# Optimization experiments

Hardware: AMD Instinct MI355X
Metric: run time of the kernel (lower is better)

Reference implementation:

```python
import jax, jax.numpy as jnp
import numpy as np

B, S, P, D, H = 2, 1024, 1024, 2048, 16
DH = D // H
QMAX = 127.0


def quantize(x):
    # per-tensor abs-max int8 quantization, matching torch quantize(bits=8)
    scale = jnp.max(jnp.abs(x)) / QMAX
    x_q = jnp.clip(jnp.round(x / scale), -128.0, 127.0).astype(jnp.int8)
    return x_q, scale


def dequantize(x_q, scale):
    return x_q.astype(jnp.float32) * scale


def setup_inputs() -> dict:
    key = jax.random.key(0)
    ks = jax.random.split(key, 12)
    sd = 1.0 / np.sqrt(D)
    inp = {
        'hidden_states': jax.random.normal(ks[0], (B, S, D), jnp.float32),
        'Wq': jax.random.normal(ks[1], (D, D), jnp.float32) * sd,
        'bq': jnp.zeros((D,), jnp.float32),
        'Wk': jax.random.normal(ks[2], (D, D), jnp.float32) * sd,
        'bk': jnp.zeros((D,), jnp.float32),
        'Wv': jax.random.normal(ks[3], (D, D), jnp.float32) * sd,
        'bv': jnp.zeros((D,), jnp.float32),
        'Wo': jax.random.normal(ks[4], (D, D), jnp.float32) * sd,
        'bo': jnp.zeros((D,), jnp.float32),
        'past_k_q': jax.random.randint(ks[5], (B, P, D), -128, 128).astype(jnp.int8),
        'past_k_scale': jnp.float32(0.03),
        'past_v_q': jax.random.randint(ks[6], (B, P, D), -128, 128).astype(jnp.int8),
        'past_v_scale': jnp.float32(0.02),
    }
    return inp


def attention(h, k, v, Wq, bq, Wo, bo):
    # standard causal MHA; query positions are offset by the cache length P
    T = k.shape[1]  # P + S
    q = (h @ Wq + bq).reshape(B, S, H, DH)
    kh = k.reshape(B, T, H, DH)
    vh = v.reshape(B, T, H, DH)
    scores = jnp.einsum('bshd,bthd->bhst', q, kh) / np.sqrt(DH)  # [B,H,S,T]
    causal = jnp.arange(T)[None, :] <= (P + jnp.arange(S))[:, None]  # [S,T]
    scores = jnp.where(causal[None, None], scores, jnp.float32(-1e30))
    attn = jax.nn.softmax(scores, axis=-1)
    out = jnp.einsum('bhst,bthd->bshd', attn, vh).reshape(B, S, D)
    return out @ Wo + bo


def reference(hidden_states, Wq, bq, Wk, bk, Wv, bv, Wo, bo,
              past_k_q, past_k_scale, past_v_q, past_v_scale):
    k = hidden_states @ Wk + bk  # [B,S,D]
    v = hidden_states @ Wv + bv
    k_q, k_scale = quantize(k)
    v_q, v_scale = quantize(v)
    # dequantize cached KV and concat along the sequence dim (dim=1)
    k_prev = dequantize(past_k_q, past_k_scale)
    v_prev = dequantize(past_v_q, past_v_scale)
    k_full = jnp.concatenate([k_prev, k], axis=1)  # [B,P+S,D]
    v_full = jnp.concatenate([v_prev, v], axis=1)
    out = attention(hidden_states, k_full, v_full, Wq, bq, Wo, bo)
    return out, k_q, k_scale, v_q, v_scale
```

## Files before the change

kernel.cpp:

```cpp
#include <hip/hip_runtime.h>

#define SOFT_SCALE 0.08838834764831845f
#define BSD 4194304
#define NELEM 4194304

typedef __attribute__((ext_vector_type(4))) float    f32x4;
typedef __attribute__((ext_vector_type(8))) short    bf16x8;
typedef __attribute__((ext_vector_type(4))) short    bf16x4;
typedef __attribute__((ext_vector_type(4))) unsigned u32x4;

__device__ __forceinline__ float bs2f(short s) {
    unsigned u = ((unsigned)(unsigned short)s) << 16;
    return __builtin_bit_cast(float, u);
}
__device__ __forceinline__ short f2bs(float f) {
    unsigned u = __builtin_bit_cast(unsigned, f);
    unsigned r = (u + 0x7fffu + ((u >> 16) & 1u)) >> 16;
    return (short)r;
}

__device__ __forceinline__ void stage16(const short* g, short* l) {
#if __has_builtin(__builtin_amdgcn_global_load_lds)
    __builtin_amdgcn_global_load_lds(
        (const __attribute__((address_space(1))) void*)g,
        (__attribute__((address_space(3))) void*)l, 16, 0, 0);
#else
    *(bf16x8*)l = *(const bf16x8*)g;
#endif
}

__global__ void probe_init(const int* __restrict__ q, float* __restrict__ scal) {
    const int lane = threadIdx.x;
    int bad = 0;
#pragma unroll
    for (int i = 0; i < 4; ++i) {
        const int v = q[i * 64 + lane];
        bad |= (v < -128 || v > 127) ? 1 : 0;
    }
    const int anybad = __any(bad);
    if (lane == 0) ((int*)scal)[2] = anybad ? 0 : 1;
    if (lane == 1) scal[0] = 0.f;
    if (lane == 2) scal[1] = 0.f;
}

__global__ void conv_bf16(const float* __restrict__ X, short* __restrict__ Y) {
    const int stride = gridDim.x * blockDim.x;
    for (int i = blockIdx.x * blockDim.x + threadIdx.x; i < NELEM / 8; i += stride) {
        const int e = i * 8;
        f32x4 a = *(const f32x4*)&X[e];
        f32x4 b = *(const f32x4*)&X[e + 4];
        bf16x8 o;
        o[0] = f2bs(a[0]); o[1] = f2bs(a[1]); o[2] = f2bs(a[2]); o[3] = f2bs(a[3]);
        o[4] = f2bs(b[0]); o[5] = f2bs(b[1]); o[6] = f2bs(b[2]); o[7] = f2bs(b[3]);
        *(bf16x8*)&Y[e] = o;
    }
}

__global__ __launch_bounds__(256) void transpose_conv(const float* __restrict__ W0,
                                                      const float* __restrict__ W1,
                                                      const float* __restrict__ W2,
                                                      short* __restrict__ WT) {
    __shared__ __align__(16) short Tl[64 * 68];
    const float* W = blockIdx.z == 0 ? W0 : (blockIdx.z == 1 ? W1 : W2);
    short* out = WT + (long)blockIdx.z * 4194304;
    const int tid = threadIdx.x;
    const int n0 = blockIdx.x * 64, k0 = blockIdx.y * 64;
#pragma unroll
    for (int i = 0; i < 4; ++i) {
        const int e = i * 1024 + tid * 4;
        const int r = e >> 6, c = e & 63;
        f32x4 f = *(const f32x4*)&W[(long)(k0 + r) * 2048 + n0 + c];
        bf16x4 s4 = { f2bs(f[0]), f2bs(f[1]), f2bs(f[2]), f2bs(f[3]) };
        *(bf16x4*)&Tl[r * 68 + c] = s4;
    }
    __syncthreads();
#pragma unroll
    for (int i = 0; i < 4; ++i) {
        const int e = i * 1024 + tid * 4;
        const int nr = e >> 6, kk = e & 63;
        bf16x4 o = { Tl[(kk + 0) * 68 + nr], Tl[(kk + 1) * 68 + nr],
                     Tl[(kk + 2) * 68 + nr], Tl[(kk + 3) * 68 + nr] };
        *(bf16x4*)&out[(long)(n0 + nr) * 2048 + k0 + kk] = o;
    }
}

__global__ void dequant_kernel(const void* __restrict__ pk, const void* __restrict__ pv,
                               const float* __restrict__ psk, const float* __restrict__ psv,
                               short* __restrict__ Kf, short* __restrict__ Vf,
                               const int* __restrict__ wsflag) {
    const int z = blockIdx.z;
    const void* src = z ? pv : pk;
    const float sc = z ? *psv : *psk;
    short* dst = z ? Vf : Kf;
    const int flag = wsflag[2];
    const int stride = gridDim.x * blockDim.x;
    for (int i = blockIdx.x * blockDim.x + threadIdx.x; i < NELEM / 8; i += stride) {
        const int e = i * 8;
        int vals[8];
        if (flag) {
            const int* s = (const int*)src + e;
            *(int4*)&vals[0] = *(const int4*)&s[0];
            *(int4*)&vals[4] = *(const int4*)&s[4];
        } else {
            const int2 wv = *(const int2*)((const char*)src + e);
#pragma unroll
            for (int j = 0; j < 4; ++j) vals[j] = (int)(signed char)(wv.x >> (8 * j));
#pragma unroll
            for (int j = 0; j < 4; ++j) vals[4 + j] = (int)(signed char)(wv.y >> (8 * j));
        }
        bf16x8 o;
#pragma unroll
        for (int j = 0; j < 8; ++j) o[j] = f2bs((float)vals[j] * sc);
        *(bf16x8*)&dst[e + ((e >> 21) << 21)] = o;
    }
}

__global__ __launch_bounds__(256, 2) void gemm_m97(
    const short* __restrict__ A,
    const short* __restrict__ Bt0, const short* __restrict__ Bt1, const short* __restrict__ Bt2,
    const float* __restrict__ bi0, const float* __restrict__ bi1, const float* __restrict__ bi2,
    void* __restrict__ o0, void* __restrict__ o1, void* __restrict__ o2,
    int mode_sgl, float scale_sgl) {
    __shared__ __align__(16) short Al[2][4096];
    __shared__ __align__(16) short Bl[2][4096];
    const int nbx = gridDim.x, nby = gridDim.y, nbz = gridDim.z;
    const int nwg = nbx * nby * nbz;
    const int orig = blockIdx.x + nbx * (blockIdx.y + nby * blockIdx.z);
    const int cpx = nwg >> 3;
    int swz = (orig & 7) * cpx + (orig >> 3);
    const int bx = swz % nbx; swz /= nbx;
    const int by = swz % nby;
    const int bz = swz / nby;

    const short* Bt   = bz == 0 ? Bt0 : (bz == 1 ? Bt1 : Bt2);
    const float* bias = bz == 0 ? bi0 : (bz == 1 ? bi1 : bi2);
    void* outp        = bz == 0 ? o0  : (bz == 1 ? o1  : o2);
    int mode; float scl;
    if (nbz == 3) { mode = (bz == 0) ? 1 : 2; scl = (bz == 0) ? SOFT_SCALE : 1.f; }
    else          { mode = mode_sgl;          scl = scale_sgl; }

    const int tid = threadIdx.x, lane = tid & 63, w = tid >> 6;
    const int wm = w >> 1, wn = w & 1, l4 = lane >> 4, ln = lane & 15;
    const int m0 = by * 128, n0 = bx * 128;

    const short* gA0 = A  + (long)(m0 + (tid >> 2)) * 2048 + (tid & 3) * 8;
    const short* gA1 = gA0 + 64 * 2048;
    const short* gB0 = Bt + (long)(n0 + (tid >> 2)) * 2048 + (tid & 3) * 8;
    const short* gB1 = gB0 + 64 * 2048;

    f32x4 acc[4][4];
#pragma unroll
    for (int mi = 0; mi < 4; ++mi)
#pragma unroll
        for (int ni = 0; ni < 4; ++ni) acc[mi][ni] = (f32x4){0, 0, 0, 0};

#define STAGE_G(buf, ko)                                   \
    do {                                                   \
        stage16(gA0 + (ko), &Al[buf][tid * 8]);            \
        stage16(gA1 + (ko), &Al[buf][2048 + tid * 8]);     \
        stage16(gB0 + (ko), &Bl[buf][tid * 8]);            \
        stage16(gB1 + (ko), &Bl[buf][2048 + tid * 8]);     \
    } while (0)

    STAGE_G(0, 0);
    asm volatile("s_waitcnt vmcnt(0)" ::: "memory");
    __syncthreads();
    int cur = 0;
    for (int kt = 0; kt < 64; ++kt) {
        if (kt < 63) STAGE_G(cur ^ 1, (kt + 1) * 32);
        bf16x8 af[4], bfr[4];
#pragma unroll
        for (int mi = 0; mi < 4; ++mi)
            af[mi] = *(const bf16x8*)&Al[cur][(wm * 64 + mi * 16 + ln) * 32 + l4 * 8];
#pragma unroll
        for (int ni = 0; ni < 4; ++ni)
            bfr[ni] = *(const bf16x8*)&Bl[cur][(wn * 64 + ni * 16 + ln) * 32 + l4 * 8];
#pragma unroll
        for (int mi = 0; mi < 4; ++mi)
#pragma unroll
            for (int ni = 0; ni < 4; ++ni)
                acc[mi][ni] = __builtin_amdgcn_mfma_f32_16x16x32_bf16(
                    af[mi], bfr[ni], acc[mi][ni], 0, 0, 0);
        asm volatile("s_waitcnt vmcnt(0)" ::: "memory");
        __syncthreads();
        cur ^= 1;
    }
#undef STAGE_G

#pragma unroll
    for (int ni = 0; ni < 4; ++ni) {
        const int gn = n0 + wn * 64 + ni * 16 + ln;
        const float bv = bias[gn];
#pragma unroll
        for (int mi = 0; mi < 4; ++mi) {
#pragma unroll
            for (int r = 0; r < 4; ++r) {
                const int gm = m0 + wm * 64 + mi * 16 + l4 * 4 + r;
                const float v = (acc[mi][ni][r] + bv) * scl;
                if (mode == 0) {
                    ((float*)outp)[(long)gm * 2048 + gn] = v;
                } else if (mode == 1) {
                    ((short*)outp)[(long)gm * 2048 + gn] = f2bs(v);
                } else {
                    const int gr = gm + 1024 + ((gm >> 10) << 10);
                    ((short*)outp)[(long)gr * 2048 + gn] = f2bs(v);
                }
            }
        }
    }
}

__global__ void absmax_kernel(const short* __restrict__ Kf, const short* __restrict__ Vf,
                              float* __restrict__ scal) {
    const int z = blockIdx.z;
    const short* src = z ? Vf : Kf;
    const int tid = threadIdx.x, lane = tid & 63, w = tid >> 6;
    float mx = 0.f;
    const int stride = gridDim.x * blockDim.x;
    for (int i = blockIdx.x * blockDim.x + tid; i < NELEM / 8; i += stride) {
        const int e = i * 8;
        const int flat = e + 2097152 + ((e >> 21) << 21);
        bf16x8 v = *(const bf16x8*)&src[flat];
#pragma unroll
        for (int j = 0; j < 8; ++j) mx = fmaxf(mx, fabsf(bs2f(v[j])));
    }
#pragma unroll
    for (int o = 32; o > 0; o >>= 1) mx = fmaxf(mx, __shfl_xor(mx, o));
    __shared__ float wred[4];
    if (lane == 0) wred[w] = mx;
    __syncthreads();
    if (tid == 0) {
        const float m2 = fmaxf(fmaxf(wred[0], wred[1]), fmaxf(wred[2], wred[3]));
        atomicMax((unsigned int*)&scal[z], __builtin_bit_cast(unsigned int, m2));
    }
}

__global__ void quantize_kernel(const short* __restrict__ Kf, const short* __restrict__ Vf,
                                const float* __restrict__ scal, float* __restrict__ out) {
    const int z = blockIdx.z;
    const short* src = z ? Vf : Kf;
    const float mx = scal[z];
    const float scale = mx * (1.f / 127.f);
    const float inv = (mx > 0.f) ? 127.f / mx : 0.f;
    const long ob = z ? (2L * BSD + 1) : (1L * BSD);
    if (blockIdx.x == 0 && threadIdx.x == 0)
        out[z ? (3L * BSD + 1) : (2L * BSD)] = scale;
    const int stride = gridDim.x * blockDim.x;
    for (int i = blockIdx.x * blockDim.x + threadIdx.x; i < NELEM; i += stride) {
        const int flat = i + 2097152 + ((i >> 21) << 21);
        const float x = bs2f(src[flat]);
        float q = rintf(x * inv);
        q = fminf(127.f, fmaxf(-128.f, q));
        out[ob + i] = q;
    }
}

__global__ __launch_bounds__(256, 2) void attn_kernel(const short* __restrict__ Q,
                                                      const short* __restrict__ Kf,
                                                      const short* __restrict__ Vf,
                                                      short* __restrict__ O) {
    __shared__ __align__(16) short Kl[64 * 136];
    __shared__ __align__(16) short Vt[128 * 72];
    const int b = blockIdx.z, h = blockIdx.y;
    const int qt = (b == 0) ? blockIdx.x : (15 - blockIdx.x);
    const int tid = threadIdx.x, w = tid >> 6, lane = tid & 63;
    const int l4 = lane >> 4, n = lane & 15;
    const int rg = tid >> 4, cg = tid & 15, stc = cg * 8;
    const int sIdx = qt * 64 + w * 16 + n;
    const int qlim = 1024 + sIdx;

    bf16x8 qf[4];
#pragma unroll
    for (int c = 0; c < 4; ++c)
        qf[c] = *(const bf16x8*)&Q[(long)(b * 1024 + sIdx) * 2048 + h * 128 + c * 32 + l4 * 8];

    f32x4 acco[8];
#pragma unroll
    for (int i = 0; i < 8; ++i) acco[i] = (f32x4){0, 0, 0, 0};
    float m_run = -1e30f, l_run = 0.f;

    const short* Kb = Kf + (long)(b * 2048) * 2048 + h * 128;
    const short* Vb = Vf + (long)(b * 2048) * 2048 + h * 128;
    const int nt = 17 + qt;

    bf16x8 kreg[4], vreg[4];
#pragma unroll
    for (int i = 0; i < 4; ++i) kreg[i] = *(const bf16x8*)&Kb[(long)(i * 16 + rg) * 2048 + stc];
#pragma unroll
    for (int i = 0; i < 4; ++i) vreg[i] = *(const bf16x8*)&Vb[(long)(rg * 4 + i) * 2048 + stc];

    for (int t = 0; t < nt; ++t) {
        const int t0 = t * 64;
        __syncthreads();
#pragma unroll
        for (int i = 0; i < 4; ++i)
            *(bf16x8*)&Kl[(i * 16 + rg) * 136 + stc] = kreg[i];
#pragma unroll
        for (int j = 0; j < 8; ++j) {
            const int d = stc + j;
            bf16x4 c4 = { vreg[0][j], vreg[1][j], vreg[2][j], vreg[3][j] };
            *(bf16x4*)&Vt[d * 72 + ((rg ^ ((d >> 3) & 7)) << 2)] = c4;
        }
        if (t + 1 < nt) {
            const int t1 = (t + 1) * 64;
#pragma unroll
            for (int i = 0; i < 4; ++i)
                kreg[i] = *(const bf16x8*)&Kb[(long)(t1 + i * 16 + rg) * 2048 + stc];
#pragma unroll
            for (int i = 0; i < 4; ++i)
                vreg[i] = *(const bf16x8*)&Vb[(long)(t1 + rg * 4 + i) * 2048 + stc];
        }
        __syncthreads();

        float p[16];
        __builtin_amdgcn_s_setprio(1);
#pragma unroll
        for (int kt = 0; kt < 4; ++kt) {
            f32x4 sc4 = (f32x4){0, 0, 0, 0};
#pragma unroll
            for (int c = 0; c < 4; ++c) {
                bf16x8 kfr = *(const bf16x8*)&Kl[(kt * 16 + n) * 136 + c * 32 + l4 * 8];
                sc4 = __builtin_amdgcn_mfma_f32_16x16x32_bf16(kfr, qf[c], sc4, 0, 0, 0);
            }
#pragma unroll
            for (int r = 0; r < 4; ++r) {
                const int kg = t0 + kt * 16 + l4 * 4 + r;
                p[kt * 4 + r] = (kg <= qlim) ? sc4[r] : -1e30f;
            }
        }
        __builtin_amdgcn_s_setprio(0);

        float tmax = p[0];
#pragma unroll
        for (int i = 1; i < 16; ++i) tmax = fmaxf(tmax, p[i]);
        tmax = fmaxf(tmax, __shfl_xor(tmax, 16));
        tmax = fmaxf(tmax, __shfl_xor(tmax, 32));
        const float mnew = fmaxf(m_run, tmax);
        const float fac = __expf(m_run - mnew);
        float tsum = 0.f;
#pragma unroll
        for (int i = 0; i < 16; ++i) { p[i] = __expf(p[i] - mnew); tsum += p[i]; }
        tsum += __shfl_xor(tsum, 16);
        tsum += __shfl_xor(tsum, 32);
        l_run = l_run * fac + tsum;
        m_run = mnew;
#pragma unroll
        for (int i = 0; i < 8; ++i) acco[i] *= fac;

        u32x4 pw0, pw1;
#pragma unroll
        for (int wd = 0; wd < 4; ++wd) {
            unsigned r0, r1;
            asm("v_cvt_pk_bf16_f32 %0, %1, %2" : "=v"(r0) : "v"(p[2 * wd]), "v"(p[2 * wd + 1]));
            asm("v_cvt_pk_bf16_f32 %0, %1, %2" : "=v"(r1) : "v"(p[8 + 2 * wd]), "v"(p[8 + 2 * wd + 1]));
            pw0[wd] = r0; pw1[wd] = r1;
        }
        bf16x8 pb[2] = { __builtin_bit_cast(bf16x8, pw0), __builtin_bit_cast(bf16x8, pw1) };

        __builtin_amdgcn_s_setprio(1);
#pragma unroll
        for (int dc = 0; dc < 8; ++dc) {
            const int d = dc * 16 + n;
            const int swd = ((d >> 3) & 7) << 2;
#pragma unroll
            for (int k32 = 0; k32 < 2; ++k32) {
                bf16x4 g0 = *(const bf16x4*)&Vt[d * 72 + (k32 * 32 + ((4 * l4) ^ swd))];
                bf16x4 g1 = *(const bf16x4*)&Vt[d * 72 + (k32 * 32 + ((16 + 4 * l4) ^ swd))];
                bf16x8 vf = { g0[0], g0[1], g0[2], g0[3], g1[0], g1[1], g1[2], g1[3] };
                acco[dc] = __builtin_amdgcn_mfma_f32_16x16x32_bf16(vf, pb[k32], acco[dc], 0, 0, 0);
            }
        }
        __builtin_amdgcn_s_setprio(0);
    }

    __syncthreads();
    const float inv = 1.f / l_run;
#pragma unroll
    for (int dc = 0; dc < 8; ++dc)
#pragma unroll
        for (int r = 0; r < 4; ++r)
            Kl[(w * 16 + n) * 136 + dc * 16 + l4 * 4 + r] = f2bs(acco[dc][r] * inv);
    __syncthreads();
#pragma unroll
    for (int i = 0; i < 4; ++i) {
        const int row = i * 4 + (lane >> 4);
        const int col = (lane & 15) * 8;
        bf16x8 ov = *(const bf16x8*)&Kl[(w * 16 + row) * 136 + col];
        *(bf16x8*)&O[(long)(b * 1024 + qt * 64 + w * 16 + row) * 2048 + h * 128 + col] = ov;
    }
}

extern "C" void kernel_launch(void* const* d_in, const int* in_sizes, int n_in,
                              void* d_out, int out_size, void* d_ws, size_t ws_size,
                              hipStream_t stream) {
    const float* h   = (const float*)d_in[0];
    const float* Wq  = (const float*)d_in[1];
    const float* bq  = (const float*)d_in[2];
    const float* Wk  = (const float*)d_in[3];
    const float* bk  = (const float*)d_in[4];
    const float* Wv  = (const float*)d_in[5];
    const float* bv  = (const float*)d_in[6];
    const float* Wo  = (const float*)d_in[7];
    const float* bo  = (const float*)d_in[8];
    const void*  pkq = d_in[9];
    const float* pks = (const float*)d_in[10];
    const void*  pvq = d_in[11];
    const float* pvs = (const float*)d_in[12];
    float* out = (float*)d_out;

    char* ws = (char*)d_ws;
    dim3 blk(256);
    dim3 tr_grid(32, 32);
    const bool big = (ws_size >= 75500000ull);

    if (big) {
        float* scal  = (float*)ws;
        short* hbf   = (short*)(ws + 256);
        short* WT3   = (short*)(ws + 256 + 1L * 8388608);
        short* Qbf   = (short*)(ws + 256 + 4L * 8388608);
        short* Kfull = (short*)(ws + 256 + 5L * 8388608);
        short* Vfull = (short*)(ws + 256 + 5L * 8388608 + 16777216);
        short* attnb = hbf;

        probe_init<<<1, 64, 0, stream>>>((const int*)pkq, scal);
        conv_bf16<<<1024, blk, 0, stream>>>(h, hbf);
        dequant_kernel<<<dim3(256, 1, 2), blk, 0, stream>>>(pkq, pvq, pks, pvs, Kfull, Vfull,
                                                            (const int*)d_ws);
        transpose_conv<<<dim3(32, 32, 3), blk, 0, stream>>>(Wq, Wk, Wv, WT3);
        gemm_m97<<<dim3(16, 16, 3), blk, 0, stream>>>(hbf, WT3, WT3 + 4194304, WT3 + 8388608,
                                                      bq, bk, bv, Qbf, Kfull, Vfull, 0, 1.f);
        absmax_kernel<<<dim3(512, 1, 2), blk, 0, stream>>>(Kfull, Vfull, scal);
        quantize_kernel<<<dim3(512, 1, 2), blk, 0, stream>>>(Kfull, Vfull, scal, out);
        attn_kernel<<<dim3(16, 16, 2), blk, 0, stream>>>(Qbf, Kfull, Vfull, attnb);
        transpose_conv<<<dim3(32, 32, 1), blk, 0, stream>>>(Wo, Wo, Wo, WT3);
        gemm_m97<<<dim3(16, 16, 1), blk, 0, stream>>>(attnb, WT3, WT3, WT3, bo, bo, bo,
                                                      out, out, out, 0, 1.f);
    } else {
        float* scal  = (float*)ws;
        short* hbf   = (short*)(ws + 256);
        short* WT    = (short*)(ws + 256 + 1L * 8388608);
        short* Qbf   = (short*)(ws + 256 + 2L * 8388608);
        short* Kfull = (short*)(ws + 256 + 3L * 8388608);
        short* Vfull = (short*)(ws + 256 + 3L * 8388608 + 16777216);
        short* attnb = hbf;

        probe_init<<<1, 64, 0, stream>>>((const int*)pkq, scal);
        conv_bf16<<<1024, blk, 0, stream>>>(h, hbf);
        dequant_kernel<<<dim3(256, 1, 2), blk, 0, stream>>>(pkq, pvq, pks, pvs, Kfull, Vfull,
                                                            (const int*)d_ws);
        transpose_conv<<<dim3(32, 32, 1), blk, 0, stream>>>(Wk, Wk, Wk, WT);
        gemm_m97<<<dim3(16, 16, 1), blk, 0, stream>>>(hbf, WT, WT, WT, bk, bk, bk,
                                                      Kfull, Kfull, Kfull, 2, 1.f);
        transpose_conv<<<dim3(32, 32, 1), blk, 0, stream>>>(Wv, Wv, Wv, WT);
        gemm_m97<<<dim3(16, 16, 1), blk, 0, stream>>>(hbf, WT, WT, WT, bv, bv, bv,
                                                      Vfull, Vfull, Vfull, 2, 1.f);
        absmax_kernel<<<dim3(512, 1, 2), blk, 0, stream>>>(Kfull, Vfull, scal);
        quantize_kernel<<<dim3(512, 1, 2), blk, 0, stream>>>(Kfull, Vfull, scal, out);
        transpose_conv<<<dim3(32, 32, 1), blk, 0, stream>>>(Wq, Wq, Wq, WT);
        gemm_m97<<<dim3(16, 16, 1), blk, 0, stream>>>(hbf, WT, WT, WT, bq, bq, bq,
                                                      Qbf, Qbf, Qbf, 1, SOFT_SCALE);
        attn_kernel<<<dim3(16, 16, 2), blk, 0, stream>>>(Qbf, Kfull, Vfull, attnb);
        transpose_conv<<<dim3(32, 32, 1), blk, 0, stream>>>(Wo, Wo, Wo, WT);
        gemm_m97<<<dim3(16, 16, 1), blk, 0, stream>>>(attnb, WT, WT, WT, bo, bo, bo,
                                                      out, out, out, 0, 1.f);
    }
}
```

Measured before the change: 237.5 us.

## Fuse absmax into GEMM epilogue, deepen GEMM pipeline, tune attention softmax

The separate absmax kernel is removed, and the K/V abs-max is now reduced in the projection GEMM epilogue with a wave shuffle plus atomicMax. The GEMM moves from double to quad LDS buffering with partial vmcnt waits, an XOR swizzle on LDS columns and s_setprio around the MFMAs. Attention gains a new block-to-(head,batch,tile) mapping, skips causal masking on early tiles, and adds a lazy online-softmax rescale with an 8.0 threshold. The quantize kernel is vectorised to four elements per thread. Quad buffering doubles GEMM LDS use, which may reduce occupancy.

```diff
diff --git a/kernel.cpp b/kernel.cpp
--- a/kernel.cpp
+++ b/kernel.cpp
@@ -120,9 +120,9 @@
     const short* __restrict__ Bt0, const short* __restrict__ Bt1, const short* __restrict__ Bt2,
     const float* __restrict__ bi0, const float* __restrict__ bi1, const float* __restrict__ bi2,
     void* __restrict__ o0, void* __restrict__ o1, void* __restrict__ o2,
-    int mode_sgl, float scale_sgl) {
-    __shared__ __align__(16) short Al[2][4096];
-    __shared__ __align__(16) short Bl[2][4096];
+    float* __restrict__ scal, int mode_sgl, float scale_sgl, int amax_sgl) {
+    __shared__ __align__(16) short Al[4][4096];
+    __shared__ __align__(16) short Bl[4][4096];
     const int nbx = gridDim.x, nby = gridDim.y, nbz = gridDim.z;
     const int nwg = nbx * nby * nbz;
     const int orig = blockIdx.x + nbx * (blockIdx.y + nby * blockIdx.z);
@@ -135,17 +135,20 @@
     const short* Bt   = bz == 0 ? Bt0 : (bz == 1 ? Bt1 : Bt2);
     const float* bias = bz == 0 ? bi0 : (bz == 1 ? bi1 : bi2);
     void* outp        = bz == 0 ? o0  : (bz == 1 ? o1  : o2);
-    int mode; float scl;
-    if (nbz == 3) { mode = (bz == 0) ? 1 : 2; scl = (bz == 0) ? SOFT_SCALE : 1.f; }
-    else          { mode = mode_sgl;          scl = scale_sgl; }
+    int mode, amx; float scl;
+    if (nbz == 3) { mode = (bz == 0) ? 1 : 2; scl = (bz == 0) ? SOFT_SCALE : 1.f;
+                    amx = (bz == 0) ? -1 : (bz - 1); }
+    else          { mode = mode_sgl; scl = scale_sgl; amx = amax_sgl; }
 
     const int tid = threadIdx.x, lane = tid & 63, w = tid >> 6;
     const int wm = w >> 1, wn = w & 1, l4 = lane >> 4, ln = lane & 15;
     const int m0 = by * 128, n0 = bx * 128;
 
-    const short* gA0 = A  + (long)(m0 + (tid >> 2)) * 2048 + (tid & 3) * 8;
+    const int srow = tid >> 2;
+    const int cswz = ((tid & 3) ^ ((srow >> 1) & 3)) * 8;
+    const short* gA0 = A  + (long)(m0 + srow) * 2048 + cswz;
     const short* gA1 = gA0 + 64 * 2048;
-    const short* gB0 = Bt + (long)(n0 + (tid >> 2)) * 2048 + (tid & 3) * 8;
+    const short* gB0 = Bt + (long)(n0 + srow) * 2048 + cswz;
     const short* gB1 = gB0 + 64 * 2048;
 
     f32x4 acc[4][4];
@@ -163,30 +166,37 @@
     } while (0)
 
     STAGE_G(0, 0);
-    asm volatile("s_waitcnt vmcnt(0)" ::: "memory");
-    __syncthreads();
-    int cur = 0;
+    STAGE_G(1, 32);
+    STAGE_G(2, 64);
+
+    const int gsw = (ln >> 1) & 3;
     for (int kt = 0; kt < 64; ++kt) {
-        if (kt < 63) STAGE_G(cur ^ 1, (kt + 1) * 32);
+        if (kt < 62)      asm volatile("s_waitcnt vmcnt(8)" ::: "memory");
+        else if (kt == 62) asm volatile("s_waitcnt vmcnt(4)" ::: "memory");
+        else               asm volatile("s_waitcnt vmcnt(0)" ::: "memory");
+        asm volatile("s_waitcnt lgkmcnt(0)" ::: "memory");
+        __builtin_amdgcn_s_barrier();
+        if (kt < 61) STAGE_G((kt + 3) & 3, (kt + 3) * 32);
+        const int cur = kt & 3;
         bf16x8 af[4], bfr[4];
 #pragma unroll
         for (int mi = 0; mi < 4; ++mi)
-            af[mi] = *(const bf16x8*)&Al[cur][(wm * 64 + mi * 16 + ln) * 32 + l4 * 8];
+            af[mi] = *(const bf16x8*)&Al[cur][(wm * 64 + mi * 16 + ln) * 32 + (l4 ^ gsw) * 8];
 #pragma unroll
         for (int ni = 0; ni < 4; ++ni)
-            bfr[ni] = *(const bf16x8*)&Bl[cur][(wn * 64 + ni * 16 + ln) * 32 + l4 * 8];
+            bfr[ni] = *(const bf16x8*)&Bl[cur][(wn * 64 + ni * 16 + ln) * 32 + (l4 ^ gsw) * 8];
+        __builtin_amdgcn_s_setprio(1);
 #pragma unroll
         for (int mi = 0; mi < 4; ++mi)
 #pragma unroll
             for (int ni = 0; ni < 4; ++ni)
                 acc[mi][ni] = __builtin_amdgcn_mfma_f32_16x16x32_bf16(
                     af[mi], bfr[ni], acc[mi][ni], 0, 0, 0);
-        asm volatile("s_waitcnt vmcnt(0)" ::: "memory");
-        __syncthreads();
-        cur ^= 1;
+        __builtin_amdgcn_s_setprio(0);
     }
 #undef STAGE_G
 
+    float amax = 0.f;
 #pragma unroll
     for (int ni = 0; ni < 4; ++ni) {
         const int gn = n0 + wn * 64 + ni * 16 + ln;
@@ -197,6 +207,7 @@
             for (int r = 0; r < 4; ++r) {
                 const int gm = m0 + wm * 64 + mi * 16 + l4 * 4 + r;
                 const float v = (acc[mi][ni][r] + bv) * scl;
+                amax = fmaxf(amax, fabsf(v));
                 if (mode == 0) {
                     ((float*)outp)[(long)gm * 2048 + gn] = v;
                 } else if (mode == 1) {
@@ -208,30 +219,11 @@
             }
         }
     }
-}
-
-__global__ void absmax_kernel(const short* __restrict__ Kf, const short* __restrict__ Vf,
-                              float* __restrict__ scal) {
-    const int z = blockIdx.z;
-    const short* src = z ? Vf : Kf;
-    const int tid = threadIdx.x, lane = tid & 63, w = tid >> 6;
-    float mx = 0.f;
-    const int stride = gridDim.x * blockDim.x;
-    for (int i = blockIdx.x * blockDim.x + tid; i < NELEM / 8; i += stride) {
-        const int e = i * 8;
-        const int flat = e + 2097152 + ((e >> 21) << 21);
-        bf16x8 v = *(const bf16x8*)&src[flat];
-#pragma unroll
-        for (int j = 0; j < 8; ++j) mx = fmaxf(mx, fabsf(bs2f(v[j])));
-    }
-#pragma unroll
-    for (int o = 32; o > 0; o >>= 1) mx = fmaxf(mx, __shfl_xor(mx, o));
-    __shared__ float wred[4];
-    if (lane == 0) wred[w] = mx;
-    __syncthreads();
-    if (tid == 0) {
-        const float m2 = fmaxf(fmaxf(wred[0], wred[1]), fmaxf(wred[2], wred[3]));
-        atomicMax((unsigned int*)&scal[z], __builtin_bit_cast(unsigned int, m2));
+    if (amx >= 0) {
+#pragma unroll
+        for (int o = 32; o > 0; o >>= 1) amax = fmaxf(amax, __shfl_xor(amax, o));
+        if (lane == 0)
+            atomicMax((unsigned int*)&scal[amx], __builtin_bit_cast(unsigned int, amax));
     }
 }
 
@@ -246,12 +238,16 @@
     if (blockIdx.x == 0 && threadIdx.x == 0)
         out[z ? (3L * BSD + 1) : (2L * BSD)] = scale;
     const int stride = gridDim.x * blockDim.x;
-    for (int i = blockIdx.x * blockDim.x + threadIdx.x; i < NELEM; i += stride) {
-        const int flat = i + 2097152 + ((i >> 21) << 21);
-        const float x = bs2f(src[flat]);
-        float q = rintf(x * inv);
-        q = fminf(127.f, fmaxf(-128.f, q));
-        out[ob + i] = q;
+    for (int i = blockIdx.x * blockDim.x + threadIdx.x; i < NELEM / 4; i += stride) {
+        const int e = i * 4;
+        const int flat = e + 2097152 + ((e >> 21) << 21);
+        bf16x4 x4 = *(const bf16x4*)&src[flat];
+        float4 q;
+        q.x = fminf(127.f, fmaxf(-128.f, rintf(bs2f(x4[0]) * inv)));
+        q.y = fminf(127.f, fmaxf(-128.f, rintf(bs2f(x4[1]) * inv)));
+        q.z = fminf(127.f, fmaxf(-128.f, rintf(bs2f(x4[2]) * inv)));
+        q.w = fminf(127.f, fmaxf(-128.f, rintf(bs2f(x4[3]) * inv)));
+        *(float4*)&out[ob + e] = q;
     }
 }
 
@@ -261,8 +257,13 @@
                                                       short* __restrict__ O) {
     __shared__ __align__(16) short Kl[64 * 136];
     __shared__ __align__(16) short Vt[128 * 72];
-    const int b = blockIdx.z, h = blockIdx.y;
-    const int qt = (b == 0) ? blockIdx.x : (15 - blockIdx.x);
+    const int L = blockIdx.x + 16 * (blockIdx.y + 16 * blockIdx.z);
+    const int x = L & 7, rr = L >> 3;
+    const int qt0 = rr & 15, pgrp = rr >> 4;
+    const int p = x + 8 * pgrp;
+    const int h = p >> 1, b = p & 1;
+    const int qt = (pgrp >= 2) ? (15 - qt0) : qt0;
+
     const int tid = threadIdx.x, w = tid >> 6, lane = tid & 63;
     const int l4 = lane >> 4, n = lane & 15;
     const int rg = tid >> 4, cg = tid & 15, stc = cg * 8;
@@ -312,7 +313,7 @@
         }
         __syncthreads();
 
-        float p[16];
+        float p16[16];
         __builtin_amdgcn_s_setprio(1);
 #pragma unroll
         for (int kt = 0; kt < 4; ++kt) {
@@ -323,36 +324,43 @@
                 sc4 = __builtin_amdgcn_mfma_f32_16x16x32_bf16(kfr, qf[c], sc4, 0, 0, 0);
             }
 #pragma unroll
-            for (int r = 0; r < 4; ++r) {
-                const int kg = t0 + kt * 16 + l4 * 4 + r;
-                p[kt * 4 + r] = (kg <= qlim) ? sc4[r] : -1e30f;
+            for (int r = 0; r < 4; ++r) p16[kt * 4 + r] = sc4[r];
+        }
+        __builtin_amdgcn_s_setprio(0);
+        if (t >= 16) {
+#pragma unroll
+            for (int i = 0; i < 16; ++i) {
+                const int kg = t0 + (i >> 2) * 16 + l4 * 4 + (i & 3);
+                if (kg > qlim) p16[i] = -1e30f;
             }
         }
-        __builtin_amdgcn_s_setprio(0);
-
-        float tmax = p[0];
-#pragma unroll
-        for (int i = 1; i < 16; ++i) tmax = fmaxf(tmax, p[i]);
+
+        float tmax = p16[0];
+#pragma unroll
+        for (int i = 1; i < 16; ++i) tmax = fmaxf(tmax, p16[i]);
         tmax = fmaxf(tmax, __shfl_xor(tmax, 16));
         tmax = fmaxf(tmax, __shfl_xor(tmax, 32));
-        const float mnew = fmaxf(m_run, tmax);
-        const float fac = __expf(m_run - mnew);
+        if (!__all(tmax <= m_run + 8.f)) {
+            const float mnew = fmaxf(m_run, tmax);
+            const float fac = __expf(m_run - mnew);
+            l_run *= fac;
+#pragma unroll
+            for (int i = 0; i < 8; ++i) acco[i] *= fac;
+            m_run = mnew;
+        }
         float tsum = 0.f;
 #pragma unroll
-        for (int i = 0; i < 16; ++i) { p[i] = __expf(p[i] - mnew); tsum += p[i]; }
+        for (int i = 0; i < 16; ++i) { p16[i] = __expf(p16[i] - m_run); tsum += p16[i]; }
         tsum += __shfl_xor(tsum, 16);
         tsum += __shfl_xor(tsum, 32);
-        l_run = l_run * fac + tsum;
-        m_run = mnew;
-#pragma unroll
-        for (int i = 0; i < 8; ++i) acco[i] *= fac;
+        l_run += tsum;
 
         u32x4 pw0, pw1;
 #pragma unroll
         for (int wd = 0; wd < 4; ++wd) {
             unsigned r0, r1;
-            asm("v_cvt_pk_bf16_f32 %0, %1, %2" : "=v"(r0) : "v"(p[2 * wd]), "v"(p[2 * wd + 1]));
-            asm("v_cvt_pk_bf16_f32 %0, %1, %2" : "=v"(r1) : "v"(p[8 + 2 * wd]), "v"(p[8 + 2 * wd + 1]));
+            asm("v_cvt_pk_bf16_f32 %0, %1, %2" : "=v"(r0) : "v"(p16[2 * wd]), "v"(p16[2 * wd + 1]));
+            asm("v_cvt_pk_bf16_f32 %0, %1, %2" : "=v"(r1) : "v"(p16[8 + 2 * wd]), "v"(p16[8 + 2 * wd + 1]));
             pw0[wd] = r0; pw1[wd] = r1;
         }
         bf16x8 pb[2] = { __builtin_bit_cast(bf16x8, pw0), __builtin_bit_cast(bf16x8, pw1) };
@@ -410,7 +418,6 @@
 
     char* ws = (char*)d_ws;
     dim3 blk(256);
-    dim3 tr_grid(32, 32);
     const bool big = (ws_size >= 75500000ull);
 
     if (big) {
@@ -428,13 +435,13 @@
                                                             (const int*)d_ws);
         transpose_conv<<<dim3(32, 32, 3), blk, 0, stream>>>(Wq, Wk, Wv, WT3);
         gemm_m97<<<dim3(16, 16, 3), blk, 0, stream>>>(hbf, WT3, WT3 + 4194304, WT3 + 8388608,
-                                                      bq, bk, bv, Qbf, Kfull, Vfull, 0, 1.f);
-        absmax_kernel<<<dim3(512, 1, 2), blk, 0, stream>>>(Kfull, Vfull, scal);
-        quantize_kernel<<<dim3(512, 1, 2), blk, 0, stream>>>(Kfull, Vfull, scal, out);
+                                                      bq, bk, bv, Qbf, Kfull, Vfull,
+                                                      scal, 0, 1.f, -1);
+        quantize_kernel<<<dim3(256, 1, 2), blk, 0, stream>>>(Kfull, Vfull, scal, out);
         attn_kernel<<<dim3(16, 16, 2), blk, 0, stream>>>(Qbf, Kfull, Vfull, attnb);
         transpose_conv<<<dim3(32, 32, 1), blk, 0, stream>>>(Wo, Wo, Wo, WT3);
         gemm_m97<<<dim3(16, 16, 1), blk, 0, stream>>>(attnb, WT3, WT3, WT3, bo, bo, bo,
-                                                      out, out, out, 0, 1.f);
+                                                      out, out, out, scal, 0, 1.f, -1);
     } else {
         float* scal  = (float*)ws;
         short* hbf   = (short*)(ws + 256);
@@ -450,18 +457,17 @@
                                                             (const int*)d_ws);
         transpose_conv<<<dim3(32, 32, 1), blk, 0, stream>>>(Wk, Wk, Wk, WT);
         gemm_m97<<<dim3(16, 16, 1), blk, 0, stream>>>(hbf, WT, WT, WT, bk, bk, bk,
-                                                      Kfull, Kfull, Kfull, 2, 1.f);
+                                                      Kfull, Kfull, Kfull, scal, 2, 1.f, 0);
         transpose_conv<<<dim3(32, 32, 1), blk, 0, stream>>>(Wv, Wv, Wv, WT);
         gemm_m97<<<dim3(16, 16, 1), blk, 0, stream>>>(hbf, WT, WT, WT, bv, bv, bv,
-                                                      Vfull, Vfull, Vfull, 2, 1.f);
-        absmax_kernel<<<dim3(512, 1, 2), blk, 0, stream>>>(Kfull, Vfull, scal);
-        quantize_kernel<<<dim3(512, 1, 2), blk, 0, stream>>>(Kfull, Vfull, scal, out);
+                                                      Vfull, Vfull, Vfull, scal, 2, 1.f, 1);
+        quantize_kernel<<<dim3(256, 1, 2), blk, 0, stream>>>(Kfull, Vfull, scal, out);
         transpose_conv<<<dim3(32, 32, 1), blk, 0, stream>>>(Wq, Wq, Wq, WT);
         gemm_m97<<<dim3(16, 16, 1), blk, 0, stream>>>(hbf, WT, WT, WT, bq, bq, bq,
-                                                      Qbf, Qbf, Qbf, 1, SOFT_SCALE);
+                                                      Qbf, Qbf, Qbf, scal, 1, SOFT_SCALE, -1);
         attn_kernel<<<dim3(16, 16, 2), blk, 0, stream>>>(Qbf, Kfull, Vfull, attnb);
         transpose_conv<<<dim3(32, 32, 1), blk, 0, stream>>>(Wo, Wo, Wo, WT);
         gemm_m97<<<dim3(16, 16, 1), blk, 0, stream>>>(attnb, WT, WT, WT, bo, bo, bo,
-                                                      out, out, out, 0, 1.f);
-    }
-}
+                                                      out, out, out, scal, 0, 1.f, -1);
+    }
+}
```

Result: slower. 263.1 us (+10.8%).
